# Kernel tuning notes

Hardware: AMD Instinct MI355X
Metric: run time of the kernel (lower is better)

## Reference

```python
import jax, jax.numpy as jnp
import numpy as np
import math

B, L, D, H = 2, 2048, 512, 8
DH = D // H  # 64
MAX_SEQ = 2048


def setup_inputs() -> dict:
    key = jax.random.key(0)
    ks = jax.random.split(key, 9)
    rn = lambda k, sh: jax.random.normal(k, sh, dtype=jnp.float32)
    w_scale = 0.02
    # causal mask: 1 where attention is disallowed (upper triangle)
    causal = jnp.triu(jnp.ones((L, L), jnp.float32), k=1)[None, None]
    return {
        "q_in": rn(ks[0], (B, L, D)),
        "k_in": rn(ks[1], (B, L, D)),
        "v_in": rn(ks[2], (B, L, D)),
        "mask": causal,
        "Wq": rn(ks[3], (D, D)) * w_scale,
        "bq": jnp.zeros((D,), jnp.float32),
        "Wk": rn(ks[4], (D, D)) * w_scale,
        "bk": jnp.zeros((D,), jnp.float32),
        "Wv": rn(ks[5], (D, D)) * w_scale,
        "bv": jnp.zeros((D,), jnp.float32),
        "Wfc": rn(ks[6], (D, D)) * w_scale,
        "bfc": jnp.zeros((D,), jnp.float32),
        "E": rn(ks[7], (MAX_SEQ, DH)),  # relative position embedding (non-trainable buffer)
    }


def _heads(x, W, b):
    # [B,L,D] -> [B,H,L,DH]
    y = x @ W + b
    return y.reshape(x.shape[0], x.shape[1], H, DH).transpose(0, 2, 1, 3)


def _qe_mask(len_q):
    # keep[l, m] = (m >= len_q - 1 - l); zeros out invalid relative offsets
    rows = jnp.arange(len_q)[:, None]
    cols = jnp.arange(len_q)[None, :]
    return (cols >= (len_q - 1 - rows)).astype(jnp.float32)


def _skew(QE):
    # Music-Transformer skewing: [B,H,L,M] -> pad left on last dim ->
    # reshape swapping last two dims -> drop first row => Srel [B,H,M,L]
    b, h, l, m = QE.shape
    padded = jnp.pad(QE, ((0, 0), (0, 0), (0, 0), (1, 0)))  # [b,h,l,m+1]
    reshaped = padded.reshape(b, h, m + 1, l)
    return reshaped[:, :, 1:, :]  # [b,h,m,l]


def reference(q_in, k_in, v_in, mask, Wq, bq, Wk, bk, Wv, bv, Wfc, bfc, E):
    q = _heads(q_in, Wq, bq)  # [B,H,L,DH]
    k = _heads(k_in, Wk, bk)
    v = _heads(v_in, Wv, bv)
    len_q = q.shape[2]
    # left embedding slice: E[max(0, MAX_SEQ - len_q):]
    e = E[max(0, MAX_SEQ - len_q):, :]  # [M, DH], M == len_q here
    QE = jnp.einsum('bhld,md->bhlm', q, e)
    QE = QE * _qe_mask(len_q)  # broadcast [L,M] over [B,H,L,M]
    Srel = _skew(QE)  # [B,H,L,L]
    QKt = jnp.einsum('bhld,bhmd->bhlm', q, k)
    logits = (QKt + Srel) / np.sqrt(DH).astype(np.float32)
    logits = logits + mask * (-1e9)
    attn_weights = jax.nn.softmax(logits, axis=-1)
    attn = jnp.einsum('bhlm,bhmd->bhld', attn_weights, v)
    out = attn.transpose(0, 2, 1, 3).reshape(q_in.shape[0], -1, D)
    out = out @ Wfc + bfc
    return out, attn_weights
```

## Files before the change

kernel.cpp:

```cpp
#include <hip/hip_runtime.h>
#include <math.h>

#define L 2048
#define DMODEL 512
#define NH 8
#define DH 64
#define NROWS 4096

typedef __attribute__((ext_vector_type(4))) float f32x4;
typedef __attribute__((ext_vector_type(8))) short s16x8;

#define MFMA(a, b, c) __builtin_amdgcn_mfma_f32_16x16x32_bf16(a, b, c, 0, 0, 0)

static __device__ __forceinline__ ushort f2b(float f) {
    union { float f; unsigned u; } v; v.f = f;
    unsigned r = v.u + 0x7FFF + ((v.u >> 16) & 1);
    return (ushort)(r >> 16);
}

__global__ __launch_bounds__(256)
void cvt_bf16(const float* __restrict__ in, ushort* __restrict__ out, int n8) {
    int i = blockIdx.x * 256 + threadIdx.x;
    if (i < n8) {
        float4 a = *reinterpret_cast<const float4*>(&in[(size_t)i * 8]);
        float4 b = *reinterpret_cast<const float4*>(&in[(size_t)i * 8 + 4]);
        ushort4 o0; o0.x = f2b(a.x); o0.y = f2b(a.y); o0.z = f2b(a.z); o0.w = f2b(a.w);
        ushort4 o1; o1.x = f2b(b.x); o1.y = f2b(b.y); o1.z = f2b(b.z); o1.w = f2b(b.w);
        *reinterpret_cast<ushort4*>(&out[(size_t)i * 8]) = o0;
        *reinterpret_cast<ushort4*>(&out[(size_t)i * 8 + 4]) = o1;
    }
}

__global__ __launch_bounds__(256)
void transpose_w(const float* __restrict__ W0, const float* __restrict__ W1,
                 const float* __restrict__ W2, const float* __restrict__ W3,
                 ushort* __restrict__ T0, ushort* __restrict__ T1,
                 ushort* __restrict__ T2, ushort* __restrict__ T3) {
    const int z = blockIdx.z;
    const float* W = z == 0 ? W0 : (z == 1 ? W1 : (z == 2 ? W2 : W3));
    ushort* T = z == 0 ? T0 : (z == 1 ? T1 : (z == 2 ? T2 : T3));
    __shared__ float Ls[64][65];
    const int tid = threadIdx.x;
    const int k0 = blockIdx.y * 64, n0 = blockIdx.x * 64;
    #pragma unroll
    for (int i = 0; i < 4; ++i) {
        int kk = (tid >> 4) + i * 16, n4 = (tid & 15) * 4;
        float4 v = *reinterpret_cast<const float4*>(&W[(size_t)(k0 + kk) * 512 + n0 + n4]);
        Ls[kk][n4] = v.x; Ls[kk][n4 + 1] = v.y; Ls[kk][n4 + 2] = v.z; Ls[kk][n4 + 3] = v.w;
    }
    __syncthreads();
    #pragma unroll
    for (int i = 0; i < 4; ++i) {
        int nn = (tid >> 4) + i * 16, k4 = (tid & 15) * 4;
        ushort4 o;
        o.x = f2b(Ls[k4 + 0][nn]); o.y = f2b(Ls[k4 + 1][nn]);
        o.z = f2b(Ls[k4 + 2][nn]); o.w = f2b(Ls[k4 + 3][nn]);
        *reinterpret_cast<ushort4*>(&T[(size_t)(n0 + nn) * 512 + k0 + k4]) = o;
    }
}

__global__ __launch_bounds__(256)
void gemm_bf16(const void* __restrict__ A0, const void* __restrict__ A1,
               const ushort* __restrict__ W0, const ushort* __restrict__ W1,
               const float* __restrict__ b0, const float* __restrict__ b1,
               void* o0, void* o1, int a_f32, int mode) {
    const int z = blockIdx.z;
    const void* A   = z == 0 ? A0 : A1;
    const ushort* Wt = z == 0 ? W0 : W1;
    const float* bias = z == 0 ? b0 : b1;
    void* outp = z == 0 ? o0 : o1;

    __shared__ ushort As[128][40];
    __shared__ ushort Bs[64][40];
    const int tid = threadIdx.x;
    const int w = tid >> 6, lane = tid & 63, g = lane >> 4, c = lane & 15;
    const int m0 = blockIdx.y * 128, n0 = blockIdx.x * 64;

    f32x4 acc[2][4];
    #pragma unroll
    for (int rs = 0; rs < 2; ++rs)
        #pragma unroll
        for (int cs = 0; cs < 4; ++cs) acc[rs][cs] = (f32x4){0.f, 0.f, 0.f, 0.f};

    float bsv[4];
    #pragma unroll
    for (int cs = 0; cs < 4; ++cs) bsv[cs] = bias[n0 + 16 * cs + c];

    for (int k0 = 0; k0 < 512; k0 += 32) {
        {
            int row = tid >> 1, kh = (tid & 1) * 16;
            if (a_f32) {
                const float* p = (const float*)A + (size_t)(m0 + row) * 512 + k0 + kh;
                ushort tmp[16];
                #pragma unroll
                for (int q4 = 0; q4 < 4; ++q4) {
                    float4 f = *reinterpret_cast<const float4*>(p + q4 * 4);
                    tmp[q4 * 4 + 0] = f2b(f.x); tmp[q4 * 4 + 1] = f2b(f.y);
                    tmp[q4 * 4 + 2] = f2b(f.z); tmp[q4 * 4 + 3] = f2b(f.w);
                }
                *reinterpret_cast<uint4*>(&As[row][kh]) = *reinterpret_cast<uint4*>(&tmp[0]);
                *reinterpret_cast<uint4*>(&As[row][kh + 8]) = *reinterpret_cast<uint4*>(&tmp[8]);
            } else {
                const ushort* p = (const ushort*)A + (size_t)(m0 + row) * 512 + k0 + kh;
                uint4 x0 = *reinterpret_cast<const uint4*>(p);
                uint4 x1 = *reinterpret_cast<const uint4*>(p + 8);
                *reinterpret_cast<uint4*>(&As[row][kh]) = x0;
                *reinterpret_cast<uint4*>(&As[row][kh + 8]) = x1;
            }
        }
        {
            int n = tid >> 2, kh = (tid & 3) * 8;
            uint4 x = *reinterpret_cast<const uint4*>(&Wt[(size_t)(n0 + n) * 512 + k0 + kh]);
            *reinterpret_cast<uint4*>(&Bs[n][kh]) = x;
        }
        __syncthreads();
        s16x8 af[2], bf[4];
        #pragma unroll
        for (int rs = 0; rs < 2; ++rs)
            af[rs] = *reinterpret_cast<const s16x8*>(&As[32 * w + 16 * rs + c][8 * g]);
        #pragma unroll
        for (int cs = 0; cs < 4; ++cs)
            bf[cs] = *reinterpret_cast<const s16x8*>(&Bs[16 * cs + c][8 * g]);
        #pragma unroll
        for (int rs = 0; rs < 2; ++rs)
            #pragma unroll
            for (int cs = 0; cs < 4; ++cs)
                acc[rs][cs] = MFMA(af[rs], bf[cs], acc[rs][cs]);
        __syncthreads();
    }
    #pragma unroll
    for (int rs = 0; rs < 2; ++rs)
        #pragma unroll
        for (int cs = 0; cs < 4; ++cs)
            #pragma unroll
            for (int r = 0; r < 4; ++r) {
                int row = m0 + 32 * w + 16 * rs + 4 * g + r;
                int n = n0 + 16 * cs + c;
                float v = acc[rs][cs][r] + bsv[cs];
                int bb = row >> 11, l = row & 2047, hh = n >> 6, dh = n & 63;
                if (mode == 0) {
                    ((float*)outp)[(size_t)row * 512 + n] = v;
                } else if (mode == 1) {
                    ((ushort*)outp)[(((size_t)bb * NH + hh) * L + l) * DH + dh] = f2b(v);
                } else {
                    ((ushort*)outp)[(((size_t)bb * NH + hh) * DH + dh) * L + l] = f2b(v);
                }
            }
}

__global__ __launch_bounds__(256, 3)
void attn(const ushort* __restrict__ qws, const ushort* __restrict__ kws,
          const ushort* __restrict__ vtg, const ushort* __restrict__ Ebf,
          float* __restrict__ attnw, ushort* __restrict__ ows,
          float* __restrict__ linvg) {
    __shared__ float Ored[4][32][68];
    __shared__ float lred[4][32];
    __shared__ float linvs[32];

    const int tid = threadIdx.x;
    const int w = tid >> 6, lane = tid & 63, g = lane >> 4, c = lane & 15;
    const int bid = blockIdx.x;
    const int bh = bid & 15;
    const int ib = 63 - (bid >> 4);
    const int b = bh >> 3, h = bh & 7;
    const int i0 = ib * 32;
    const int nt = ib + 1;

    const ushort* qb = qws + (size_t)bh * L * DH;
    const ushort* kb = kws + (size_t)bh * L * DH;
    const ushort* vt = vtg + (size_t)bh * DH * L;
    float* ab = attnw + (size_t)bh * L * L;

    ushort (*Pw)[40] = reinterpret_cast<ushort(*)[40]>(&Ored[w][0][0]);

    s16x8 aq[2][2];
    #pragma unroll
    for (int rs = 0; rs < 2; ++rs)
        #pragma unroll
        for (int ks = 0; ks < 2; ++ks)
            aq[rs][ks] = *reinterpret_cast<const s16x8*>(
                qb + (size_t)(i0 + 16 * rs + c) * DH + 32 * ks + 8 * g);

    f32x4 O[2][4];
    #pragma unroll
    for (int rs = 0; rs < 2; ++rs)
        #pragma unroll
        for (int cs = 0; cs < 4; ++cs) O[rs][cs] = (f32x4){0.f, 0.f, 0.f, 0.f};
    float lsum[2][4] = {};

    for (int t = w; t < nt; t += 4) {
        const int j0 = t * 32;
        const int rbase = L - 32 - i0 + j0;

        f32x4 TT[4][2];
        #pragma unroll
        for (int ct = 0; ct < 4; ++ct) {
            s16x8 be[2];
            int rg = rbase + 16 * ct + c;
            rg = rg > L - 1 ? L - 1 : rg;
            #pragma unroll
            for (int ks = 0; ks < 2; ++ks)
                be[ks] = *reinterpret_cast<const s16x8*>(
                    Ebf + (size_t)rg * DH + 32 * ks + 8 * g);
            #pragma unroll
            for (int rs = 0; rs < 2; ++rs) {
                f32x4 x = {0.f, 0.f, 0.f, 0.f};
                x = MFMA(aq[rs][0], be[0], x);
                x = MFMA(aq[rs][1], be[1], x);
                TT[ct][rs] = x;
            }
        }
        float rel[2][2][4];
        #pragma unroll
        for (int r = 0; r < 4; ++r) {
            const int u = c - 4 * g - r;
            const int src = (lane & 48) | ((15 + u) & 15);
            const bool hi = (u >= 1);
            #pragma unroll
            for (int rs = 0; rs < 2; ++rs)
                #pragma unroll
                for (int jh = 0; jh < 2; ++jh) {
                    const int b0 = jh - rs + 1;
                    float va = __shfl(TT[b0][rs][r], src);
                    float vb = __shfl(TT[b0 + 1][rs][r], src);
                    rel[rs][jh][r] = hi ? vb : va;
                }
        }
        f32x4 SK[2][2];
        {
            s16x8 bk[2][2];
            #pragma unroll
            for (int jh = 0; jh < 2; ++jh)
                #pragma unroll
                for (int ks = 0; ks < 2; ++ks)
                    bk[jh][ks] = *reinterpret_cast<const s16x8*>(
                        kb + (size_t)(j0 + 16 * jh + c) * DH + 32 * ks + 8 * g);
            #pragma unroll
            for (int rs = 0; rs < 2; ++rs)
                #pragma unroll
                for (int jh = 0; jh < 2; ++jh) {
                    f32x4 x = {0.f, 0.f, 0.f, 0.f};
                    x = MFMA(aq[rs][0], bk[jh][0], x);
                    x = MFMA(aq[rs][1], bk[jh][1], x);
                    SK[rs][jh] = x;
                }
        }
        #pragma unroll
        for (int rs = 0; rs < 2; ++rs)
            #pragma unroll
            for (int jh = 0; jh < 2; ++jh)
                #pragma unroll
                for (int r = 0; r < 4; ++r) {
                    const int il = 16 * rs + 4 * g + r;
                    const int jl = 16 * jh + c;
                    float s = (SK[rs][jh][r] + rel[rs][jh][r]) * 0.125f;
                    float p = (j0 + jl <= i0 + il) ? __expf(s) : 0.0f;
                    lsum[rs][r] += p;
                    ab[(size_t)(i0 + il) * L + j0 + jl] = p;
                    Pw[il][jl] = f2b(p);
                }
        s16x8 pa[2];
        #pragma unroll
        for (int rs2 = 0; rs2 < 2; ++rs2)
            pa[rs2] = *reinterpret_cast<const s16x8*>(&Pw[16 * rs2 + c][8 * g]);
        #pragma unroll
        for (int cs = 0; cs < 4; ++cs) {
            s16x8 vtb = *reinterpret_cast<const s16x8*>(
                vt + (size_t)(16 * cs + c) * L + j0 + 8 * g);
            #pragma unroll
            for (int rs2 = 0; rs2 < 2; ++rs2)
                O[rs2][cs] = MFMA(pa[rs2], vtb, O[rs2][cs]);
        }
    }

    #pragma unroll
    for (int rs = 0; rs < 2; ++rs)
        #pragma unroll
        for (int r = 0; r < 4; ++r) {
            float s = lsum[rs][r];
            s += __shfl_xor(s, 1); s += __shfl_xor(s, 2);
            s += __shfl_xor(s, 4); s += __shfl_xor(s, 8);
            if (c == 0) lred[w][16 * rs + 4 * g + r] = s;
        }
    #pragma unroll
    for (int rs2 = 0; rs2 < 2; ++rs2)
        #pragma unroll
        for (int cs = 0; cs < 4; ++cs)
            #pragma unroll
            for (int r = 0; r < 4; ++r)
                Ored[w][16 * rs2 + 4 * g + r][16 * cs + c] = O[rs2][cs][r];
    __syncthreads();
    if (tid < 32) {
        float l = lred[0][tid] + lred[1][tid] + lred[2][tid] + lred[3][tid];
        float inv = 1.0f / l;
        linvs[tid] = inv;
        linvg[(size_t)bh * L + i0 + tid] = inv;
    }
    __syncthreads();
    {
        const int i = tid >> 3, d8 = (tid & 7) * 8;
        const float inv = linvs[i];
        ushort o[8];
        #pragma unroll
        for (int e = 0; e < 8; ++e) {
            float a = Ored[0][i][d8 + e] + Ored[1][i][d8 + e]
                    + Ored[2][i][d8 + e] + Ored[3][i][d8 + e];
            o[e] = f2b(a * inv);
        }
        *reinterpret_cast<uint4*>(
            &ows[((size_t)b * L + i0 + i) * DMODEL + h * DH + d8]) =
            *reinterpret_cast<const uint4*>(&o[0]);
    }
}

__global__ __launch_bounds__(256)
void rescale(float* __restrict__ attnw, const float* __restrict__ linvg) {
    const int blk = blockIdx.x;
    const int bh = blk >> 11, i = blk & 2047;
    const float inv = linvg[(size_t)bh * L + i];
    float* rowp = attnw + ((size_t)bh * L + i) * L;
    const int c8 = threadIdx.x * 8;
    float4 a, b2;
    if (c8 <= i) {
        a  = *reinterpret_cast<const float4*>(rowp + c8);
        b2 = *reinterpret_cast<const float4*>(rowp + c8 + 4);
        a.x  = (c8 + 0 <= i) ? a.x  * inv : 0.f;
        a.y  = (c8 + 1 <= i) ? a.y  * inv : 0.f;
        a.z  = (c8 + 2 <= i) ? a.z  * inv : 0.f;
        a.w  = (c8 + 3 <= i) ? a.w  * inv : 0.f;
        b2.x = (c8 + 4 <= i) ? b2.x * inv : 0.f;
        b2.y = (c8 + 5 <= i) ? b2.y * inv : 0.f;
        b2.z = (c8 + 6 <= i) ? b2.z * inv : 0.f;
        b2.w = (c8 + 7 <= i) ? b2.w * inv : 0.f;
    } else {
        a = make_float4(0.f, 0.f, 0.f, 0.f);
        b2 = a;
    }
    *reinterpret_cast<float4*>(rowp + c8) = a;
    *reinterpret_cast<float4*>(rowp + c8 + 4) = b2;
}

extern "C" void kernel_launch(void* const* d_in, const int* in_sizes, int n_in,
                              void* d_out, int out_size, void* d_ws, size_t ws_size,
                              hipStream_t stream) {
    const float* q_in = (const float*)d_in[0];
    const float* k_in = (const float*)d_in[1];
    const float* v_in = (const float*)d_in[2];
    const float* Wq  = (const float*)d_in[4];
    const float* bq  = (const float*)d_in[5];
    const float* Wk  = (const float*)d_in[6];
    const float* bk  = (const float*)d_in[7];
    const float* Wv  = (const float*)d_in[8];
    const float* bv  = (const float*)d_in[9];
    const float* Wfc = (const float*)d_in[10];
    const float* bfc = (const float*)d_in[11];
    const float* E   = (const float*)d_in[12];

    float* out0  = (float*)d_out;
    float* attnw = out0 + (size_t)2 * L * DMODEL;

    const size_t NA = (size_t)NROWS * DMODEL;
    ushort* ws = (ushort*)d_ws;
    ushort* Ebf  = ws;
    ushort* Wqt  = Ebf + (size_t)L * DH;
    ushort* Wkt  = Wqt + 262144;
    ushort* Wvt  = Wkt + 262144;
    ushort* Wfct = Wvt + 262144;
    ushort* qws  = Wfct + 262144;
    ushort* kws  = qws + NA;
    ushort* vtg  = kws + NA;
    ushort* ows  = vtg + NA;
    float*  linvg = (float*)(ows + NA);

    cvt_bf16<<<dim3(64), 256, 0, stream>>>(E, Ebf, (int)(L * DH / 8));
    transpose_w<<<dim3(8, 8, 4), 256, 0, stream>>>(Wq, Wk, Wv, Wfc, Wqt, Wkt, Wvt, Wfct);
    gemm_bf16<<<dim3(8, 32, 2), 256, 0, stream>>>(q_in, k_in, Wqt, Wkt,
                                                  bq, bk, qws, kws, 1, 1);
    gemm_bf16<<<dim3(8, 32, 1), 256, 0, stream>>>(v_in, v_in, Wvt, Wvt,
                                                  bv, bv, vtg, vtg, 1, 2);
    attn<<<dim3(1024), 256, 0, stream>>>(qws, kws, vtg, Ebf, attnw, ows, linvg);
    rescale<<<dim3(32768), 256, 0, stream>>>(attnw, linvg);
    gemm_bf16<<<dim3(8, 32, 1), 256, 0, stream>>>(ows, ows, Wfct, Wfct,
                                                  bfc, bfc, out0, out0, 0, 0);
}
```

Measured before the change: 216.1 us.

## Use two-pass softmax in attention to write normalized weights and drop rescale kernel

The attention kernel now makes a first pass over key tiles to compute row sums of exp(scores), then a second pass that recomputes the scores and writes normalized probabilities directly. Those probabilities are staged through shared memory so the global stores are coalesced, and the kernel zero-fills the masked upper region itself. This removes the separate rescale kernel that read and rewrote the whole 2048x2048 weight matrix per head, at the cost of computing QK^T and QE twice. The Q/K/V projection GEMMs are merged into one launch, and the attention occupancy hint is raised from 3 to 4.

```diff
diff --git a/kernel.cpp b/kernel.cpp
--- a/kernel.cpp
+++ b/kernel.cpp
@@ -61,14 +61,18 @@
 
 __global__ __launch_bounds__(256)
 void gemm_bf16(const void* __restrict__ A0, const void* __restrict__ A1,
+               const void* __restrict__ A2,
                const ushort* __restrict__ W0, const ushort* __restrict__ W1,
+               const ushort* __restrict__ W2,
                const float* __restrict__ b0, const float* __restrict__ b1,
-               void* o0, void* o1, int a_f32, int mode) {
+               const float* __restrict__ b2,
+               void* o0, void* o1, void* o2, int a_f32, int modes) {
     const int z = blockIdx.z;
-    const void* A   = z == 0 ? A0 : A1;
-    const ushort* Wt = z == 0 ? W0 : W1;
-    const float* bias = z == 0 ? b0 : b1;
-    void* outp = z == 0 ? o0 : o1;
+    const void* A   = z == 0 ? A0 : (z == 1 ? A1 : A2);
+    const ushort* Wt = z == 0 ? W0 : (z == 1 ? W1 : W2);
+    const float* bias = z == 0 ? b0 : (z == 1 ? b1 : b2);
+    void* outp = z == 0 ? o0 : (z == 1 ? o1 : o2);
+    const int mode = (modes >> (4 * z)) & 15;
 
     __shared__ ushort As[128][40];
     __shared__ ushort Bs[64][40];
@@ -148,12 +152,11 @@
             }
 }
 
-__global__ __launch_bounds__(256, 3)
+__global__ __launch_bounds__(256, 4)
 void attn(const ushort* __restrict__ qws, const ushort* __restrict__ kws,
           const ushort* __restrict__ vtg, const ushort* __restrict__ Ebf,
-          float* __restrict__ attnw, ushort* __restrict__ ows,
-          float* __restrict__ linvg) {
-    __shared__ float Ored[4][32][68];
+          float* __restrict__ attnw, ushort* __restrict__ ows) {
+    __shared__ float Wsc[4][32][68];
     __shared__ float lred[4][32];
     __shared__ float linvs[32];
 
@@ -171,7 +174,8 @@
     const ushort* vt = vtg + (size_t)bh * DH * L;
     float* ab = attnw + (size_t)bh * L * L;
 
-    ushort (*Pw)[40] = reinterpret_cast<ushort(*)[40]>(&Ored[w][0][0]);
+    float*  Ps = &Wsc[w][0][0];
+    ushort* Pw = (ushort*)(Ps + 32 * 36);
 
     s16x8 aq[2][2];
     #pragma unroll
@@ -181,32 +185,20 @@
             aq[rs][ks] = *reinterpret_cast<const s16x8*>(
                 qb + (size_t)(i0 + 16 * rs + c) * DH + 32 * ks + 8 * g);
 
-    f32x4 O[2][4];
-    #pragma unroll
-    for (int rs = 0; rs < 2; ++rs)
-        #pragma unroll
-        for (int cs = 0; cs < 4; ++cs) O[rs][cs] = (f32x4){0.f, 0.f, 0.f, 0.f};
-    float lsum[2][4] = {};
-
-    for (int t = w; t < nt; t += 4) {
-        const int j0 = t * 32;
+    auto computeS = [&](int j0, float (&sv)[2][2][4]) {
         const int rbase = L - 32 - i0 + j0;
-
         f32x4 TT[4][2];
         #pragma unroll
         for (int ct = 0; ct < 4; ++ct) {
-            s16x8 be[2];
             int rg = rbase + 16 * ct + c;
             rg = rg > L - 1 ? L - 1 : rg;
-            #pragma unroll
-            for (int ks = 0; ks < 2; ++ks)
-                be[ks] = *reinterpret_cast<const s16x8*>(
-                    Ebf + (size_t)rg * DH + 32 * ks + 8 * g);
+            s16x8 be0 = *reinterpret_cast<const s16x8*>(Ebf + (size_t)rg * DH + 8 * g);
+            s16x8 be1 = *reinterpret_cast<const s16x8*>(Ebf + (size_t)rg * DH + 32 + 8 * g);
             #pragma unroll
             for (int rs = 0; rs < 2; ++rs) {
                 f32x4 x = {0.f, 0.f, 0.f, 0.f};
-                x = MFMA(aq[rs][0], be[0], x);
-                x = MFMA(aq[rs][1], be[1], x);
+                x = MFMA(aq[rs][0], be0, x);
+                x = MFMA(aq[rs][1], be1, x);
                 TT[ct][rs] = x;
             }
         }
@@ -226,53 +218,42 @@
                     rel[rs][jh][r] = hi ? vb : va;
                 }
         }
-        f32x4 SK[2][2];
-        {
-            s16x8 bk[2][2];
-            #pragma unroll
-            for (int jh = 0; jh < 2; ++jh)
-                #pragma unroll
-                for (int ks = 0; ks < 2; ++ks)
-                    bk[jh][ks] = *reinterpret_cast<const s16x8*>(
-                        kb + (size_t)(j0 + 16 * jh + c) * DH + 32 * ks + 8 * g);
-            #pragma unroll
-            for (int rs = 0; rs < 2; ++rs)
-                #pragma unroll
-                for (int jh = 0; jh < 2; ++jh) {
-                    f32x4 x = {0.f, 0.f, 0.f, 0.f};
-                    x = MFMA(aq[rs][0], bk[jh][0], x);
-                    x = MFMA(aq[rs][1], bk[jh][1], x);
-                    SK[rs][jh] = x;
-                }
-        }
-        #pragma unroll
-        for (int rs = 0; rs < 2; ++rs)
-            #pragma unroll
-            for (int jh = 0; jh < 2; ++jh)
+        s16x8 bk[2][2];
+        #pragma unroll
+        for (int jh = 0; jh < 2; ++jh)
+            #pragma unroll
+            for (int ks = 0; ks < 2; ++ks)
+                bk[jh][ks] = *reinterpret_cast<const s16x8*>(
+                    kb + (size_t)(j0 + 16 * jh + c) * DH + 32 * ks + 8 * g);
+        #pragma unroll
+        for (int rs = 0; rs < 2; ++rs)
+            #pragma unroll
+            for (int jh = 0; jh < 2; ++jh) {
+                f32x4 x = {0.f, 0.f, 0.f, 0.f};
+                x = MFMA(aq[rs][0], bk[jh][0], x);
+                x = MFMA(aq[rs][1], bk[jh][1], x);
                 #pragma unroll
                 for (int r = 0; r < 4; ++r) {
                     const int il = 16 * rs + 4 * g + r;
                     const int jl = 16 * jh + c;
-                    float s = (SK[rs][jh][r] + rel[rs][jh][r]) * 0.125f;
-                    float p = (j0 + jl <= i0 + il) ? __expf(s) : 0.0f;
-                    lsum[rs][r] += p;
-                    ab[(size_t)(i0 + il) * L + j0 + jl] = p;
-                    Pw[il][jl] = f2b(p);
-                }
-        s16x8 pa[2];
-        #pragma unroll
-        for (int rs2 = 0; rs2 < 2; ++rs2)
-            pa[rs2] = *reinterpret_cast<const s16x8*>(&Pw[16 * rs2 + c][8 * g]);
-        #pragma unroll
-        for (int cs = 0; cs < 4; ++cs) {
-            s16x8 vtb = *reinterpret_cast<const s16x8*>(
-                vt + (size_t)(16 * cs + c) * L + j0 + 8 * g);
-            #pragma unroll
-            for (int rs2 = 0; rs2 < 2; ++rs2)
-                O[rs2][cs] = MFMA(pa[rs2], vtb, O[rs2][cs]);
-        }
-    }
-
+                    float s = (x[r] + rel[rs][jh][r]) * 0.125f;
+                    sv[rs][jh][r] = (j0 + jl <= i0 + il) ? s : -1.0e30f;
+                }
+            }
+    };
+
+    float lsum[2][4] = {};
+    for (int t = w; t < nt; t += 4) {
+        float sv[2][2][4];
+        computeS(t * 32, sv);
+        #pragma unroll
+        for (int rs = 0; rs < 2; ++rs)
+            #pragma unroll
+            for (int jh = 0; jh < 2; ++jh)
+                #pragma unroll
+                for (int r = 0; r < 4; ++r)
+                    lsum[rs][r] += __expf(sv[rs][jh][r]);
+    }
     #pragma unroll
     for (int rs = 0; rs < 2; ++rs)
         #pragma unroll
@@ -282,62 +263,91 @@
             s += __shfl_xor(s, 4); s += __shfl_xor(s, 8);
             if (c == 0) lred[w][16 * rs + 4 * g + r] = s;
         }
+    __syncthreads();
+    if (tid < 32)
+        linvs[tid] = 1.0f / (lred[0][tid] + lred[1][tid] + lred[2][tid] + lred[3][tid]);
+    __syncthreads();
+    float myi[2][4];
+    #pragma unroll
+    for (int rs = 0; rs < 2; ++rs)
+        #pragma unroll
+        for (int r = 0; r < 4; ++r)
+            myi[rs][r] = linvs[16 * rs + 4 * g + r];
+
+    f32x4 O[2][4];
+    #pragma unroll
+    for (int rs = 0; rs < 2; ++rs)
+        #pragma unroll
+        for (int cs = 0; cs < 4; ++cs) O[rs][cs] = (f32x4){0.f, 0.f, 0.f, 0.f};
+
+    for (int t = w; t < nt; t += 4) {
+        const int j0 = t * 32;
+        float sv[2][2][4];
+        computeS(j0, sv);
+        #pragma unroll
+        for (int rs = 0; rs < 2; ++rs)
+            #pragma unroll
+            for (int jh = 0; jh < 2; ++jh)
+                #pragma unroll
+                for (int r = 0; r < 4; ++r) {
+                    const int il = 16 * rs + 4 * g + r;
+                    const int jl = 16 * jh + c;
+                    float p = __expf(sv[rs][jh][r]) * myi[rs][r];
+                    Ps[il * 36 + jl] = p;
+                    Pw[il * 40 + jl] = f2b(p);
+                }
+        {
+            const int row = lane >> 1, cb = (lane & 1) * 16;
+            float* dst = &ab[(size_t)(i0 + row) * L + j0 + cb];
+            const float* srcp = &Ps[row * 36 + cb];
+            #pragma unroll
+            for (int e = 0; e < 4; ++e)
+                *reinterpret_cast<float4*>(dst + 4 * e) =
+                    *reinterpret_cast<const float4*>(srcp + 4 * e);
+        }
+        s16x8 pa[2];
+        #pragma unroll
+        for (int rs2 = 0; rs2 < 2; ++rs2)
+            pa[rs2] = *reinterpret_cast<const s16x8*>(&Pw[(16 * rs2 + c) * 40 + 8 * g]);
+        #pragma unroll
+        for (int cs = 0; cs < 4; ++cs) {
+            s16x8 vtb = *reinterpret_cast<const s16x8*>(
+                vt + (size_t)(16 * cs + c) * L + j0 + 8 * g);
+            #pragma unroll
+            for (int rs2 = 0; rs2 < 2; ++rs2)
+                O[rs2][cs] = MFMA(pa[rs2], vtb, O[rs2][cs]);
+        }
+    }
+
     #pragma unroll
     for (int rs2 = 0; rs2 < 2; ++rs2)
         #pragma unroll
         for (int cs = 0; cs < 4; ++cs)
             #pragma unroll
             for (int r = 0; r < 4; ++r)
-                Ored[w][16 * rs2 + 4 * g + r][16 * cs + c] = O[rs2][cs][r];
-    __syncthreads();
-    if (tid < 32) {
-        float l = lred[0][tid] + lred[1][tid] + lred[2][tid] + lred[3][tid];
-        float inv = 1.0f / l;
-        linvs[tid] = inv;
-        linvg[(size_t)bh * L + i0 + tid] = inv;
-    }
+                Wsc[w][16 * rs2 + 4 * g + r][16 * cs + c] = O[rs2][cs][r];
     __syncthreads();
     {
         const int i = tid >> 3, d8 = (tid & 7) * 8;
-        const float inv = linvs[i];
         ushort o[8];
         #pragma unroll
         for (int e = 0; e < 8; ++e) {
-            float a = Ored[0][i][d8 + e] + Ored[1][i][d8 + e]
-                    + Ored[2][i][d8 + e] + Ored[3][i][d8 + e];
-            o[e] = f2b(a * inv);
+            float a = Wsc[0][i][d8 + e] + Wsc[1][i][d8 + e]
+                    + Wsc[2][i][d8 + e] + Wsc[3][i][d8 + e];
+            o[e] = f2b(a);
         }
         *reinterpret_cast<uint4*>(
             &ows[((size_t)b * L + i0 + i) * DMODEL + h * DH + d8]) =
             *reinterpret_cast<const uint4*>(&o[0]);
     }
-}
-
-__global__ __launch_bounds__(256)
-void rescale(float* __restrict__ attnw, const float* __restrict__ linvg) {
-    const int blk = blockIdx.x;
-    const int bh = blk >> 11, i = blk & 2047;
-    const float inv = linvg[(size_t)bh * L + i];
-    float* rowp = attnw + ((size_t)bh * L + i) * L;
-    const int c8 = threadIdx.x * 8;
-    float4 a, b2;
-    if (c8 <= i) {
-        a  = *reinterpret_cast<const float4*>(rowp + c8);
-        b2 = *reinterpret_cast<const float4*>(rowp + c8 + 4);
-        a.x  = (c8 + 0 <= i) ? a.x  * inv : 0.f;
-        a.y  = (c8 + 1 <= i) ? a.y  * inv : 0.f;
-        a.z  = (c8 + 2 <= i) ? a.z  * inv : 0.f;
-        a.w  = (c8 + 3 <= i) ? a.w  * inv : 0.f;
-        b2.x = (c8 + 4 <= i) ? b2.x * inv : 0.f;
-        b2.y = (c8 + 5 <= i) ? b2.y * inv : 0.f;
-        b2.z = (c8 + 6 <= i) ? b2.z * inv : 0.f;
-        b2.w = (c8 + 7 <= i) ? b2.w * inv : 0.f;
-    } else {
-        a = make_float4(0.f, 0.f, 0.f, 0.f);
-        b2 = a;
-    }
-    *reinterpret_cast<float4*>(rowp + c8) = a;
-    *reinterpret_cast<float4*>(rowp + c8 + 4) = b2;
+
+    {
+        const int row = tid >> 3, cj = (tid & 7) * 4;
+        const float4 z = make_float4(0.f, 0.f, 0.f, 0.f);
+        float* rowp = &ab[(size_t)(i0 + row) * L];
+        for (int j0z = nt * 32; j0z < L; j0z += 32)
+            *reinterpret_cast<float4*>(rowp + j0z + cj) = z;
+    }
 }
 
 extern "C" void kernel_launch(void* const* d_in, const int* in_sizes, int n_in,
@@ -370,16 +380,14 @@
     ushort* kws  = qws + NA;
     ushort* vtg  = kws + NA;
     ushort* ows  = vtg + NA;
-    float*  linvg = (float*)(ows + NA);
 
     cvt_bf16<<<dim3(64), 256, 0, stream>>>(E, Ebf, (int)(L * DH / 8));
     transpose_w<<<dim3(8, 8, 4), 256, 0, stream>>>(Wq, Wk, Wv, Wfc, Wqt, Wkt, Wvt, Wfct);
-    gemm_bf16<<<dim3(8, 32, 2), 256, 0, stream>>>(q_in, k_in, Wqt, Wkt,
-                                                  bq, bk, qws, kws, 1, 1);
-    gemm_bf16<<<dim3(8, 32, 1), 256, 0, stream>>>(v_in, v_in, Wvt, Wvt,
-                                                  bv, bv, vtg, vtg, 1, 2);
-    attn<<<dim3(1024), 256, 0, stream>>>(qws, kws, vtg, Ebf, attnw, ows, linvg);
-    rescale<<<dim3(32768), 256, 0, stream>>>(attnw, linvg);
-    gemm_bf16<<<dim3(8, 32, 1), 256, 0, stream>>>(ows, ows, Wfct, Wfct,
-                                                  bfc, bfc, out0, out0, 0, 0);
-}
+    gemm_bf16<<<dim3(8, 32, 3), 256, 0, stream>>>(q_in, k_in, v_in, Wqt, Wkt, Wvt,
+                                                  bq, bk, bv, qws, kws, vtg,
+                                                  1, 0x211);
+    attn<<<dim3(1024), 256, 0, stream>>>(qws, kws, vtg, Ebf, attnw, ows);
+    gemm_bf16<<<dim3(8, 32, 1), 256, 0, stream>>>(ows, ows, ows, Wfct, Wfct, Wfct,
+                                                  bfc, bfc, bfc, out0, out0, out0,
+                                                  0, 0x0);
+}
```

Measured after the change: 228.4 us. 1.06x slower.
